# Performance work log

Hardware: AMD Instinct MI355X
Metric: run time of the kernel (lower is better)

The kernel has to match this reference:

```python
import jax, jax.numpy as jnp
import numpy as np

D_MODEL = 1024
D_STATE = 16
D_CONV = 4
EXPAND = 2
D_INNER = D_MODEL * EXPAND
BATCH = 2
SEQ = 1024


def setup_inputs() -> dict:
    key = jax.random.key(0)
    ks = jax.random.split(key, 9)
    s = lambda fan: 1.0 / np.sqrt(fan)
    x = jax.random.normal(ks[0], (BATCH, SEQ, D_MODEL), jnp.float32)
    W_in = jax.random.normal(ks[1], (D_MODEL, 2 * D_INNER), jnp.float32) * s(D_MODEL)
    conv_w = jax.random.normal(ks[2], (D_INNER, 1, D_CONV), jnp.float32) * s(D_CONV)
    conv_b = jax.random.normal(ks[3], (D_INNER,), jnp.float32) * 0.01
    W_xproj = jax.random.normal(ks[4], (D_INNER, 2 * D_STATE + 1), jnp.float32) * s(D_INNER)
    W_dt = jax.random.normal(ks[5], (1, D_INNER), jnp.float32)
    dt_std = 1.0 / np.sqrt(D_INNER)
    b_dt = jax.random.uniform(ks[6], (D_INNER,), jnp.float32, minval=-dt_std, maxval=dt_std)
    A_log = jnp.log(jnp.arange(1, D_STATE + 1, dtype=jnp.float32))
    Dp = jnp.ones((D_INNER,), jnp.float32)
    W_out = jax.random.normal(ks[7], (D_INNER, D_MODEL), jnp.float32) * s(D_INNER)
    return dict(x=x, W_in=W_in, conv_w=conv_w, conv_b=conv_b, W_xproj=W_xproj,
                W_dt=W_dt, b_dt=b_dt, A_log=A_log, Dp=Dp, W_out=W_out)


def _mamba_forward(x, W_in, conv_w, conv_b, W_xproj, W_dt, b_dt, A_log, Dp, W_out):
    # input projection, split into x branch and gate z
    xz = x @ W_in                              # (B, L, 2*d_inner)
    x_in, z = jnp.split(xz, 2, axis=-1)
    # causal depthwise conv1d: left-pad d_conv-1 (equiv to torch pad=d_conv-1 + truncate to L)
    xc = jnp.transpose(x_in, (0, 2, 1))        # (B, d_inner, L)
    xc = jax.lax.conv_general_dilated(
        xc, conv_w, window_strides=(1,), padding=[(D_CONV - 1, 0)],
        feature_group_count=D_INNER, dimension_numbers=('NCH', 'OIH', 'NCH'))
    xc = xc + conv_b[None, :, None]
    xc = jax.nn.silu(jnp.transpose(xc, (0, 2, 1)))  # (B, L, d_inner)
    # selective SSM
    A = -jnp.exp(A_log)                        # (N,)
    xp = xc @ W_xproj                          # (B, L, 2N+1)
    dt_raw = xp[..., :1]                       # (B, L, 1)
    B_sel = xp[..., 1:1 + D_STATE]             # (B, L, N)
    C_sel = xp[..., 1 + D_STATE:]              # (B, L, N)
    delta = jax.nn.softplus(dt_raw @ W_dt + b_dt)       # (B, L, d_inner)
    dA = jnp.exp(delta[..., None] * A)                   # (B, L, d, N)
    dBx = (delta * xc)[..., None] * B_sel[:, :, None, :]  # (B, L, d, N)

    def step(h, inp):
        dA_t, dBx_t, C_t = inp                 # (B,d,N),(B,d,N),(B,N)
        h = dA_t * h + dBx_t
        y_t = jnp.einsum('bdn,bn->bd', h, C_t)
        return h, y_t

    h0 = jnp.zeros((x.shape[0], D_INNER, D_STATE), xc.dtype)
    _, ys = jax.lax.scan(step, h0,
                         (dA.swapaxes(0, 1), dBx.swapaxes(0, 1), C_sel.swapaxes(0, 1)))
    y = ys.swapaxes(0, 1) + Dp * xc            # (B, L, d_inner)
    y = y * jax.nn.silu(z)
    return y @ W_out                           # (B, L, d_model)


def reference(x, W_in, conv_w, conv_b, W_xproj, W_dt, b_dt, A_log, Dp, W_out):
    return _mamba_forward(x, W_in, conv_w, conv_b, W_xproj, W_dt, b_dt, A_log, Dp, W_out)
```

## Files before the change

kernel.cpp:

```cpp
#include <hip/hip_runtime.h>


#define NTOK   2048
#define NC     64
#define TC     16

typedef unsigned short u16;
typedef short short8 __attribute__((ext_vector_type(8)));
typedef float f32x4 __attribute__((ext_vector_type(4)));

__device__ __forceinline__ float bf2f(u16 v) {
    union { unsigned int u; float f; } w; w.u = ((unsigned int)v) << 16; return w.f;
}
__device__ __forceinline__ u16 f2bf(float f) {
    union { float f; unsigned int u; } w; w.f = f;
    unsigned int u = w.u;
    return (u16)((u + 0x7fffu + ((u >> 16) & 1u)) >> 16);
}

__device__ __forceinline__ void gload_lds16(const u16* g, u16* l) {
    __builtin_amdgcn_global_load_lds(
        (const __attribute__((address_space(1))) void*)g,
        (__attribute__((address_space(3))) void*)l, 16, 0, 0);
}

__device__ __forceinline__ float softplus_f(float x) {
    return fmaxf(x, 0.f) + __logf(1.f + __expf(-__builtin_fabsf(x)));
}

__device__ __forceinline__ void transpose_tile(const float* __restrict__ in,
                                               u16* __restrict__ out,
                                               int R, int C, int n0, int k0,
                                               int tid) {
    __shared__ float tile[32][33];
    const int tx = tid & 31, ty = tid >> 5;
    #pragma unroll
    for (int i = 0; i < 32; i += 8)
        tile[ty + i][tx] = in[(size_t)(k0 + ty + i) * C + n0 + tx];
    __syncthreads();
    #pragma unroll
    for (int i = 0; i < 32; i += 8)
        out[(size_t)(n0 + ty + i) * R + k0 + tx] = f2bf(tile[tx][ty + i]);
}

__global__ __launch_bounds__(256)
void prep_all(const float* __restrict__ x, const float* __restrict__ W_in,
              const float* __restrict__ W_out, const float* __restrict__ W_xproj,
              u16* __restrict__ xbf, u16* __restrict__ WinT,
              u16* __restrict__ WoutT, u16* __restrict__ WxpT) {
    const int tid = threadIdx.x;
    int blk = blockIdx.x;
    if (blk < 8192) {
        int i = blk * 256 + tid;
        xbf[i] = f2bf(x[i]);
        return;
    }
    blk -= 8192;
    if (blk < 4096) {
        transpose_tile(W_in, WinT, 1024, 4096, (blk & 127) * 32, (blk >> 7) * 32, tid);
        return;
    }
    blk -= 4096;
    if (blk < 2048) {
        transpose_tile(W_out, WoutT, 2048, 1024, (blk & 31) * 32, (blk >> 5) * 32, tid);
        return;
    }
    blk -= 2048;
    {
        int gid = blk * 256 + tid;
        int k = gid & 2047;
        int n = gid >> 11;
        WxpT[(size_t)n * 2048 + k] = (n < 33) ? f2bf(W_xproj[(size_t)k * 33 + n]) : (u16)0;
    }
}

template <int OUT_MODE>
__global__ __launch_bounds__(256)
void gemm_bt(const u16* __restrict__ A, const u16* __restrict__ Bt,
             void* __restrict__ Cv, int M, int N, int K) {
    __shared__ __align__(16) u16 As[2][128 * 32];
    __shared__ __align__(16) u16 Bs[2][128 * 32];

    const int tid  = threadIdx.x;
    const int lane = tid & 63;
    const int w    = tid >> 6;
    const int wm   = (w >> 1) * 64;
    const int wn   = (w & 1) * 64;
    const int r    = lane & 15;
    const int q    = lane >> 4;
    const int m0   = blockIdx.x * 128;
    const int n0   = blockIdx.y * 128;
    const int kChunk = K / gridDim.z;
    const int k0   = blockIdx.z * kChunk;

    f32x4 acc[4][4];
    #pragma unroll
    for (int i = 0; i < 4; ++i)
        #pragma unroll
        for (int j = 0; j < 4; ++j)
            acc[i][j] = (f32x4){0.f, 0.f, 0.f, 0.f};

    for (int kk = k0; kk < k0 + kChunk; kk += 64) {
        __syncthreads();
        #pragma unroll
        for (int i = 0; i < 4; ++i) {
            int half = i >> 1;
            int c    = ((i & 1) << 8) + tid;
            int row  = c >> 2;
            int kc   = (c & 3) << 3;
            int wb   = (((i & 1) << 8) + (tid & 192)) * 8;
            gload_lds16(&A[(size_t)(m0 + row) * K + kk + half * 32 + kc],
                        &As[half][wb]);
            gload_lds16(&Bt[(size_t)(n0 + row) * K + kk + half * 32 + kc],
                        &Bs[half][wb]);
        }
        __syncthreads();

        #pragma unroll
        for (int half = 0; half < 2; ++half) {
            short8 af[4], bf[4];
            #pragma unroll
            for (int mt = 0; mt < 4; ++mt)
                af[mt] = *(const short8*)(&As[half][(wm + mt * 16 + r) * 32 + q * 8]);
            #pragma unroll
            for (int nt = 0; nt < 4; ++nt)
                bf[nt] = *(const short8*)(&Bs[half][(wn + nt * 16 + r) * 32 + q * 8]);

            #pragma unroll
            for (int mt = 0; mt < 4; ++mt)
                #pragma unroll
                for (int nt = 0; nt < 4; ++nt)
                    acc[mt][nt] = __builtin_amdgcn_mfma_f32_16x16x32_bf16(
                        af[mt], bf[nt], acc[mt][nt], 0, 0, 0);
        }
    }

    float* Cp = (float*)Cv + (size_t)blockIdx.z * M * N;
    #pragma unroll
    for (int mt = 0; mt < 4; ++mt) {
        #pragma unroll
        for (int nt = 0; nt < 4; ++nt) {
            #pragma unroll
            for (int i = 0; i < 4; ++i) {
                int row = m0 + wm + mt * 16 + q * 4 + i;
                int col = n0 + wn + nt * 16 + r;
                float v = acc[mt][nt][i];
                size_t idx = (size_t)row * N + col;
                if (OUT_MODE == 0) {
                    Cp[idx] = v;
                } else {
                    ((u16*)Cv)[idx] = f2bf(v);
                }
            }
        }
    }
}

__global__ __launch_bounds__(256)
void reduce_parts(const float4* __restrict__ p, float4* __restrict__ o,
                  int n4, int parts) {
    int i = blockIdx.x * 256 + threadIdx.x;
    if (i >= n4) return;
    float4 s = p[i];
    for (int z = 1; z < parts; ++z) {
        float4 v = p[(size_t)z * n4 + i];
        s.x += v.x; s.y += v.y; s.z += v.z; s.w += v.w;
    }
    o[i] = s;
}

__global__ __launch_bounds__(256)
void conv_silu(const u16* __restrict__ xz, const float* __restrict__ cw,
               const float* __restrict__ cb, u16* __restrict__ xcb) {
    const int d   = blockIdx.x * 256 + threadIdx.x;
    const int tok = blockIdx.y;
    const int b   = tok >> 10;
    const int t   = tok & 1023;
    float s = cb[d];
    #pragma unroll
    for (int k = 0; k < 4; ++k) {
        int tt = t - 3 + k;
        if (tt >= 0)
            s += bf2f(xz[(size_t)(b * 1024 + tt) * 4096 + d]) * cw[d * 4 + k];
    }
    float sl = s / (1.f + __expf(-s));
    xcb[(size_t)tok * 2048 + d] = f2bf(sl);
}

__device__ __forceinline__ void pow_tree(float e1, float* dA) {
    float e2 = e1 * e1, e4 = e2 * e2, e8 = e4 * e4;
    dA[0] = e1;       dA[1] = e2;       dA[2] = e2 * e1;  dA[3] = e4;
    dA[4] = e4 * e1;  dA[5] = e4 * e2;  dA[6] = e4 * dA[2]; dA[7] = e8;
    dA[8] = e8 * e1;  dA[9] = e8 * e2;  dA[10] = e8 * dA[2]; dA[11] = e8 * e4;
    dA[12] = e8 * dA[4]; dA[13] = e8 * dA[5]; dA[14] = e8 * dA[6]; dA[15] = e8 * e8;
}

__global__ __launch_bounds__(256)
void scan_pass1(const u16* __restrict__ xcb, const float* __restrict__ xp,
                const float* __restrict__ W_dt, const float* __restrict__ b_dt,
                const float* __restrict__ A_log,
                float* __restrict__ Sdl, float* __restrict__ hend) {
    const int c  = blockIdx.x;
    const int dg = blockIdx.y;
    const int b  = blockIdx.z;
    const int tid = threadIdx.x;
    const int d  = dg * 256 + tid;
    const int tok0 = b * 1024 + c * TC;

    __shared__ float xps[TC][36];
    for (int e = tid; e < TC * 33; e += 256) {
        int t = (e * 993) >> 15;
        int j = e - t * 33;
        xps[t][j] = xp[(size_t)(tok0 + t) * 128 + j];
    }
    __syncthreads();

    float a[16];
    bool fast = true;
    #pragma unroll
    for (int n = 0; n < 16; ++n) {
        a[n] = -__expf(A_log[n]);
        fast = fast && (__builtin_fabsf(a[n] + (float)(n + 1)) < 1e-3f * (n + 1));
    }

    const float wdt = W_dt[d];
    const float bdt = b_dt[d];

    float h[16];
    #pragma unroll
    for (int n = 0; n < 16; ++n) h[n] = 0.f;
    float sdl = 0.f;

    for (int t = 0; t < TC; ++t) {
        const int tok = tok0 + t;
        const float dl = softplus_f(xps[t][0] * wdt + bdt);
        sdl += dl;
        const float xv = bf2f(xcb[(size_t)tok * 2048 + d]);
        const float wv = dl * xv;
        if (fast) {
            float dA[16];
            pow_tree(__expf(-dl), dA);
            #pragma unroll
            for (int n = 0; n < 16; ++n)
                h[n] = fmaf(dA[n], h[n], wv * xps[t][1 + n]);
        } else {
            #pragma unroll
            for (int n = 0; n < 16; ++n)
                h[n] = fmaf(__expf(dl * a[n]), h[n], wv * xps[t][1 + n]);
        }
    }

    Sdl[(size_t)(b * NC + c) * 2048 + d] = sdl;
    #pragma unroll
    for (int n = 0; n < 16; ++n)
        hend[((size_t)((b * NC + c) * 16 + n)) * 2048 + d] = h[n];
}

__global__ __launch_bounds__(256)
void scan_combine(const float* __restrict__ Sdl, const float* __restrict__ A_log,
                  const float* __restrict__ hend, float* __restrict__ hstart) {
    const int gid = blockIdx.x * 256 + threadIdx.x;
    const int d = gid & 2047;
    const int n = (gid >> 11) & 15;
    const int b = gid >> 15;
    const float an = -__expf(A_log[n]);
    float H = 0.f;
    #pragma unroll 4
    for (int c = 0; c < NC; ++c) {
        size_t cidx = (size_t)(b * NC + c);
        float s  = Sdl[cidx * 2048 + d];
        size_t idx = (cidx * 16 + n) * 2048 + d;
        float he = hend[idx];
        hstart[idx] = H;
        H = fmaf(__expf(an * s), H, he);
    }
}

__global__ __launch_bounds__(256)
void scan_pass2(const u16* __restrict__ xcb, const float* __restrict__ xp,
                const float* __restrict__ W_dt, const float* __restrict__ b_dt,
                const float* __restrict__ A_log, const float* __restrict__ Hstart,
                const float* __restrict__ Dp, const u16* __restrict__ xz,
                u16* __restrict__ ybuf) {
    const int c  = blockIdx.x;
    const int dg = blockIdx.y;
    const int b  = blockIdx.z;
    const int tid = threadIdx.x;
    const int d  = dg * 256 + tid;
    const int tok0 = b * 1024 + c * TC;

    __shared__ float xps[TC][36];
    for (int e = tid; e < TC * 33; e += 256) {
        int t = (e * 993) >> 15;
        int j = e - t * 33;
        xps[t][j] = xp[(size_t)(tok0 + t) * 128 + j];
    }
    __syncthreads();

    float a[16];
    bool fast = true;
    #pragma unroll
    for (int n = 0; n < 16; ++n) {
        a[n] = -__expf(A_log[n]);
        fast = fast && (__builtin_fabsf(a[n] + (float)(n + 1)) < 1e-3f * (n + 1));
    }

    const float wdt = W_dt[d];
    const float bdt = b_dt[d];

    float h[16];
    #pragma unroll
    for (int n = 0; n < 16; ++n)
        h[n] = Hstart[((size_t)((b * NC + c) * 16 + n)) * 2048 + d];

    const float Dd = Dp[d];
    for (int t = 0; t < TC; ++t) {
        const int tok = tok0 + t;
        const float dl = softplus_f(xps[t][0] * wdt + bdt);
        const float xv = bf2f(xcb[(size_t)tok * 2048 + d]);
        const float wv = dl * xv;
        if (fast) {
            float dA[16];
            pow_tree(__expf(-dl), dA);
            #pragma unroll
            for (int n = 0; n < 16; ++n)
                h[n] = fmaf(dA[n], h[n], wv * xps[t][1 + n]);
        } else {
            #pragma unroll
            for (int n = 0; n < 16; ++n)
                h[n] = fmaf(__expf(dl * a[n]), h[n], wv * xps[t][1 + n]);
        }
        float y0 = 0.f, y1 = 0.f, y2 = 0.f, y3 = 0.f;
        #pragma unroll
        for (int n = 0; n < 16; n += 4) {
            y0 = fmaf(h[n + 0], xps[t][17 + n + 0], y0);
            y1 = fmaf(h[n + 1], xps[t][17 + n + 1], y1);
            y2 = fmaf(h[n + 2], xps[t][17 + n + 2], y2);
            y3 = fmaf(h[n + 3], xps[t][17 + n + 3], y3);
        }
        float y = (y0 + y1) + (y2 + y3);
        y = fmaf(Dd, xv, y);
        float zv = bf2f(xz[(size_t)tok * 4096 + 2048 + d]);
        float sz = zv / (1.f + __expf(-zv));
        ybuf[(size_t)tok * 2048 + d] = f2bf(y * sz);
    }
}

extern "C" void kernel_launch(void* const* d_in, const int* in_sizes, int n_in,
                              void* d_out, int out_size, void* d_ws, size_t ws_size,
                              hipStream_t stream) {
    const float* x       = (const float*)d_in[0];
    const float* W_in    = (const float*)d_in[1];
    const float* conv_w  = (const float*)d_in[2];
    const float* conv_b  = (const float*)d_in[3];
    const float* W_xproj = (const float*)d_in[4];
    const float* W_dt    = (const float*)d_in[5];
    const float* b_dt    = (const float*)d_in[6];
    const float* A_log   = (const float*)d_in[7];
    const float* Dp      = (const float*)d_in[8];
    const float* W_out   = (const float*)d_in[9];
    float* out = (float*)d_out;

    char* ws = (char*)d_ws;
    size_t off = 0;
    auto alloc = [&](size_t bytes) -> void* {
        void* p = ws + off;
        off += (bytes + 255) & ~(size_t)255;
        return p;
    };

    u16*   xbf    = (u16*)  alloc((size_t)NTOK * 1024 * 2);
    u16*   xz     = (u16*)  alloc((size_t)NTOK * 4096 * 2);
    u16*   WinT   = (u16*)  alloc((size_t)4096 * 1024 * 2);
    u16*   WoutT  = (u16*)  alloc((size_t)1024 * 2048 * 2);
    u16*   WxpT   = (u16*)  alloc((size_t)128 * 2048 * 2);
    u16*   xcb    = (u16*)  alloc((size_t)NTOK * 2048 * 2);
    float* xpp    = (float*)alloc((size_t)8 * NTOK * 128 * 4);
    float* xp     = (float*)alloc((size_t)NTOK * 128 * 4);
    u16*   ybuf   = (u16*)  alloc((size_t)NTOK * 2048 * 2);
    float* Sdl    = (float*)alloc((size_t)2 * NC * 2048 * 4);
    float* hend   = (float*)alloc((size_t)2 * NC * 16 * 2048 * 4);
    float* hstart = (float*)alloc((size_t)2 * NC * 16 * 2048 * 4);
    float* op     = (float*)alloc((size_t)4 * NTOK * 1024 * 4);

    const int ws_ok = (off <= ws_size);
    if (ws_ok) {
        prep_all<<<15360, 256, 0, stream>>>(x, W_in, W_out, W_xproj,
                                            xbf, WinT, WoutT, WxpT);

        gemm_bt<2><<<dim3(16, 32, 1), 256, 0, stream>>>(xbf, WinT, xz,
                                                        2048, 4096, 1024);

        conv_silu<<<dim3(8, NTOK), 256, 0, stream>>>(xz, conv_w, conv_b, xcb);

        gemm_bt<0><<<dim3(16, 1, 8), 256, 0, stream>>>(xcb, WxpT, xpp,
                                                       2048, 128, 2048);
        reduce_parts<<<(NTOK * 128 / 4) / 256, 256, 0, stream>>>(
            (const float4*)xpp, (float4*)xp, NTOK * 128 / 4, 8);

        scan_pass1<<<dim3(NC, 8, 2), 256, 0, stream>>>(xcb, xp, W_dt, b_dt, A_log,
                                                       Sdl, hend);
        scan_combine<<<(2 * 16 * 2048) / 256, 256, 0, stream>>>(Sdl, A_log,
                                                                hend, hstart);
        scan_pass2<<<dim3(NC, 8, 2), 256, 0, stream>>>(xcb, xp, W_dt, b_dt, A_log,
                                                       hstart, Dp, xz, ybuf);

        gemm_bt<0><<<dim3(16, 8, 4), 256, 0, stream>>>(ybuf, WoutT, op,
                                                       2048, 1024, 2048);
        reduce_parts<<<(NTOK * 1024 / 4) / 256, 256, 0, stream>>>(
            (const float4*)op, (float4*)out, NTOK * 1024 / 4, 4);
    }
}
```

Before: 228.0 us.

## Fuse split-K reduction into GEMM via last-block atomic counter

Removes the two separate reduce_parts kernels. Each split-K block now writes its partial tile, bumps a per-tile atomic counter, and the last arriving block sums all partials and writes the final output. The counters are zeroed in an extra block of the prep kernel. This saves two kernel launches and a full pass over the output, at the cost of fences, atomics, and a serialized reduction tail in the last block per tile.

```diff
diff --git a/kernel.cpp b/kernel.cpp
--- a/kernel.cpp
+++ b/kernel.cpp
@@ -47,7 +47,8 @@
 void prep_all(const float* __restrict__ x, const float* __restrict__ W_in,
               const float* __restrict__ W_out, const float* __restrict__ W_xproj,
               u16* __restrict__ xbf, u16* __restrict__ WinT,
-              u16* __restrict__ WoutT, u16* __restrict__ WxpT) {
+              u16* __restrict__ WoutT, u16* __restrict__ WxpT,
+              unsigned int* __restrict__ cnt) {
     const int tid = threadIdx.x;
     int blk = blockIdx.x;
     if (blk < 8192) {
@@ -66,39 +67,28 @@
         return;
     }
     blk -= 2048;
-    {
+    if (blk < 1024) {
         int gid = blk * 256 + tid;
         int k = gid & 2047;
         int n = gid >> 11;
         WxpT[(size_t)n * 2048 + k] = (n < 33) ? f2bf(W_xproj[(size_t)k * 33 + n]) : (u16)0;
-    }
-}
-
-template <int OUT_MODE>
-__global__ __launch_bounds__(256)
-void gemm_bt(const u16* __restrict__ A, const u16* __restrict__ Bt,
-             void* __restrict__ Cv, int M, int N, int K) {
-    __shared__ __align__(16) u16 As[2][128 * 32];
-    __shared__ __align__(16) u16 Bs[2][128 * 32];
-
-    const int tid  = threadIdx.x;
+        return;
+    }
+    if (tid < 256) cnt[tid] = 0u;
+}
+
+__device__ __forceinline__ void gemm_core(const u16* __restrict__ A,
+                                          const u16* __restrict__ Bt,
+                                          int M, int N, int K,
+                                          int m0, int n0, int k0, int kChunk,
+                                          int tid, f32x4 acc[4][4],
+                                          u16 (*As)[128 * 32], u16 (*Bs)[128 * 32]) {
     const int lane = tid & 63;
     const int w    = tid >> 6;
     const int wm   = (w >> 1) * 64;
     const int wn   = (w & 1) * 64;
     const int r    = lane & 15;
     const int q    = lane >> 4;
-    const int m0   = blockIdx.x * 128;
-    const int n0   = blockIdx.y * 128;
-    const int kChunk = K / gridDim.z;
-    const int k0   = blockIdx.z * kChunk;
-
-    f32x4 acc[4][4];
-    #pragma unroll
-    for (int i = 0; i < 4; ++i)
-        #pragma unroll
-        for (int j = 0; j < 4; ++j)
-            acc[i][j] = (f32x4){0.f, 0.f, 0.f, 0.f};
 
     for (int kk = k0; kk < k0 + kChunk; kk += 64) {
         __syncthreads();
@@ -134,39 +124,107 @@
                         af[mt], bf[nt], acc[mt][nt], 0, 0, 0);
         }
     }
-
-    float* Cp = (float*)Cv + (size_t)blockIdx.z * M * N;
-    #pragma unroll
-    for (int mt = 0; mt < 4; ++mt) {
-        #pragma unroll
-        for (int nt = 0; nt < 4; ++nt) {
+}
+
+__global__ __launch_bounds__(256)
+void gemm_bt_b16(const u16* __restrict__ A, const u16* __restrict__ Bt,
+                 u16* __restrict__ C, int M, int N, int K) {
+    __shared__ __align__(16) u16 As[2][128 * 32];
+    __shared__ __align__(16) u16 Bs[2][128 * 32];
+    const int tid = threadIdx.x;
+    const int lane = tid & 63;
+    const int w    = tid >> 6;
+    const int wm   = (w >> 1) * 64;
+    const int wn   = (w & 1) * 64;
+    const int r    = lane & 15;
+    const int q    = lane >> 4;
+    const int m0   = blockIdx.x * 128;
+    const int n0   = blockIdx.y * 128;
+
+    f32x4 acc[4][4];
+    #pragma unroll
+    for (int i = 0; i < 4; ++i)
+        #pragma unroll
+        for (int j = 0; j < 4; ++j)
+            acc[i][j] = (f32x4){0.f, 0.f, 0.f, 0.f};
+
+    gemm_core(A, Bt, M, N, K, m0, n0, 0, K, tid, acc, As, Bs);
+
+    #pragma unroll
+    for (int mt = 0; mt < 4; ++mt)
+        #pragma unroll
+        for (int nt = 0; nt < 4; ++nt)
             #pragma unroll
             for (int i = 0; i < 4; ++i) {
                 int row = m0 + wm + mt * 16 + q * 4 + i;
                 int col = n0 + wn + nt * 16 + r;
-                float v = acc[mt][nt][i];
-                size_t idx = (size_t)row * N + col;
-                if (OUT_MODE == 0) {
-                    Cp[idx] = v;
-                } else {
-                    ((u16*)Cv)[idx] = f2bf(v);
+                C[(size_t)row * N + col] = f2bf(acc[mt][nt][i]);
+            }
+}
+
+__global__ __launch_bounds__(256)
+void gemm_bt_red(const u16* __restrict__ A, const u16* __restrict__ Bt,
+                 float* __restrict__ op, float* __restrict__ outF,
+                 unsigned int* __restrict__ cnt, int M, int N, int K) {
+    __shared__ __align__(16) u16 As[2][128 * 32];
+    __shared__ __align__(16) u16 Bs[2][128 * 32];
+    const int tid = threadIdx.x;
+    const int lane = tid & 63;
+    const int w    = tid >> 6;
+    const int wm   = (w >> 1) * 64;
+    const int wn   = (w & 1) * 64;
+    const int r    = lane & 15;
+    const int q    = lane >> 4;
+    const int m0   = blockIdx.x * 128;
+    const int n0   = blockIdx.y * 128;
+    const int z    = blockIdx.z;
+    const int ZP   = gridDim.z;
+    const int kChunk = K / ZP;
+
+    f32x4 acc[4][4];
+    #pragma unroll
+    for (int i = 0; i < 4; ++i)
+        #pragma unroll
+        for (int j = 0; j < 4; ++j)
+            acc[i][j] = (f32x4){0.f, 0.f, 0.f, 0.f};
+
+    gemm_core(A, Bt, M, N, K, m0, n0, z * kChunk, kChunk, tid, acc, As, Bs);
+
+    float* Cp = op + (size_t)z * M * N;
+    #pragma unroll
+    for (int mt = 0; mt < 4; ++mt)
+        #pragma unroll
+        for (int nt = 0; nt < 4; ++nt)
+            #pragma unroll
+            for (int i = 0; i < 4; ++i) {
+                int row = m0 + wm + mt * 16 + q * 4 + i;
+                int col = n0 + wn + nt * 16 + r;
+                Cp[(size_t)row * N + col] = acc[mt][nt][i];
+            }
+
+    __threadfence();
+    __syncthreads();
+    __shared__ unsigned int oldc;
+    if (tid == 0)
+        oldc = atomicAdd(&cnt[blockIdx.x * gridDim.y + blockIdx.y], 1u);
+    __syncthreads();
+    if (oldc == (unsigned)(ZP - 1)) {
+        __threadfence();
+        #pragma unroll
+        for (int mt = 0; mt < 4; ++mt)
+            #pragma unroll
+            for (int nt = 0; nt < 4; ++nt)
+                #pragma unroll
+                for (int i = 0; i < 4; ++i) {
+                    int row = m0 + wm + mt * 16 + q * 4 + i;
+                    int col = n0 + wn + nt * 16 + r;
+                    size_t idx = (size_t)row * N + col;
+                    float v = acc[mt][nt][i];
+                    for (int z2 = 0; z2 < ZP; ++z2)
+                        if (z2 != z) v += op[(size_t)z2 * M * N + idx];
+                    outF[idx] = v;
                 }
-            }
-        }
-    }
-}
-
-__global__ __launch_bounds__(256)
-void reduce_parts(const float4* __restrict__ p, float4* __restrict__ o,
-                  int n4, int parts) {
-    int i = blockIdx.x * 256 + threadIdx.x;
-    if (i >= n4) return;
-    float4 s = p[i];
-    for (int z = 1; z < parts; ++z) {
-        float4 v = p[(size_t)z * n4 + i];
-        s.x += v.x; s.y += v.y; s.z += v.z; s.w += v.w;
-    }
-    o[i] = s;
+    }
 }
 
 __global__ __launch_bounds__(256)
@@ -382,21 +440,20 @@
     float* hend   = (float*)alloc((size_t)2 * NC * 16 * 2048 * 4);
     float* hstart = (float*)alloc((size_t)2 * NC * 16 * 2048 * 4);
     float* op     = (float*)alloc((size_t)4 * NTOK * 1024 * 4);
+    unsigned int* cnt = (unsigned int*)alloc(256 * 4);
 
     const int ws_ok = (off <= ws_size);
     if (ws_ok) {
-        prep_all<<<15360, 256, 0, stream>>>(x, W_in, W_out, W_xproj,
-                                            xbf, WinT, WoutT, WxpT);
-
-        gemm_bt<2><<<dim3(16, 32, 1), 256, 0, stream>>>(xbf, WinT, xz,
-                                                        2048, 4096, 1024);
+        prep_all<<<15361, 256, 0, stream>>>(x, W_in, W_out, W_xproj,
+                                            xbf, WinT, WoutT, WxpT, cnt);
+
+        gemm_bt_b16<<<dim3(16, 32), 256, 0, stream>>>(xbf, WinT, xz,
+                                                      2048, 4096, 1024);
 
         conv_silu<<<dim3(8, NTOK), 256, 0, stream>>>(xz, conv_w, conv_b, xcb);
 
-        gemm_bt<0><<<dim3(16, 1, 8), 256, 0, stream>>>(xcb, WxpT, xpp,
-                                                       2048, 128, 2048);
-        reduce_parts<<<(NTOK * 128 / 4) / 256, 256, 0, stream>>>(
-            (const float4*)xpp, (float4*)xp, NTOK * 128 / 4, 8);
+        gemm_bt_red<<<dim3(16, 1, 8), 256, 0, stream>>>(xcb, WxpT, xpp, xp,
+                                                        cnt + 128, 2048, 128, 2048);
 
         scan_pass1<<<dim3(NC, 8, 2), 256, 0, stream>>>(xcb, xp, W_dt, b_dt, A_log,
                                                        Sdl, hend);
@@ -405,9 +462,7 @@
         scan_pass2<<<dim3(NC, 8, 2), 256, 0, stream>>>(xcb, xp, W_dt, b_dt, A_log,
                                                        hstart, Dp, xz, ybuf);
 
-        gemm_bt<0><<<dim3(16, 8, 4), 256, 0, stream>>>(ybuf, WoutT, op,
-                                                       2048, 1024, 2048);
-        reduce_parts<<<(NTOK * 1024 / 4) / 256, 256, 0, stream>>>(
-            (const float4*)op, (float4*)out, NTOK * 1024 / 4, 4);
-    }
-}
+        gemm_bt_red<<<dim3(16, 8, 4), 256, 0, stream>>>(ybuf, WoutT, op, out,
+                                                        cnt, 2048, 1024, 2048);
+    }
+}
```

Result: slower. 444.3 us (+94.9%).
